# Optimization experiments

Measured on AMD Instinct MI355X. Metric: run time of the kernel, lower is better.

The kernel has to match this reference:

```python
import jax, jax.numpy as jnp
import numpy as np

B, I, O, N = 32, 512, 512, 16
XLO, XHI = 0.0, 1.0
SIGMA_INIT = (XHI - XLO) / N / 3.0
INV_SQRT2 = 0.7071067811865476


def setup_inputs() -> dict:
    key = jax.random.key(0)
    k0, k1, k2, k3, k4, k5 = jax.random.split(key, 6)
    x = jax.random.uniform(k0, (B, I), dtype=jnp.float32)  # inputs in xrange
    # learned parameters (perturbed around the module's init values so the
    # basis functions / gradients are non-degenerate)
    mx_train = 0.1 * jax.random.normal(k1, (I, O), dtype=jnp.float32)
    scale = 1.0 + 0.1 * jax.random.normal(k2, (I, O), dtype=jnp.float32)
    sigma = SIGMA_INIT * (1.0 + 0.1 * jax.random.normal(k3, (I, O, N), dtype=jnp.float32))
    alpha = 0.5 * jax.random.normal(k4, (I, O, N), dtype=jnp.float32)
    w = 0.001 * jax.random.normal(k5, (I, O, N), dtype=jnp.float32)
    # registered buffer: fixed basis centers
    mx_start = jnp.linspace(XLO, XHI, N, dtype=jnp.float32)  # (N,)
    return {"x": x, "mx_train": mx_train, "scale": scale, "sigma": sigma,
            "alpha": alpha, "w": w, "mx_start": mx_start}


def reference(x, mx_train, scale, sigma, alpha, w, mx_start):
    # z: (B, I, O, N) skewed/scaled basis argument
    centers = jnp.abs(scale)[:, :, None] * mx_start + mx_train[:, :, None]  # (I,O,N)
    z = (x[:, :, None, None] - centers[None]) / (jnp.abs(sigma) + 1e-8)
    # order == 1 branch: f = exp(-z^2) * 2*Phi(alpha*z); 2*Phi(u) = 1 + erf(u/sqrt(2))
    f = jnp.exp(-z * z) * (1.0 + jax.lax.erf(alpha * z * INV_SQRT2))
    # sum over input_dim (axis 1) and basis index n (axis 3)
    return jnp.einsum('bion,ion->bo', f, w)
```

## Files before the change

kernel.cpp:

```cpp
#include <hip/hip_runtime.h>
#include <math.h>

#define BB 32
#define II 512
#define OO 512
#define NN 16

#define NW 2
#define LOMAX (NN - NW)
#define QS 16
#define CHI 32
#define OPB 2
#define NOB (OO / OPB)

#if __has_builtin(__builtin_amdgcn_exp2f)
#define EXP2F(x) __builtin_amdgcn_exp2f(x)
#else
#define EXP2F(x) exp2f(x)
#endif
#if __has_builtin(__builtin_amdgcn_rcpf)
#define RCPF(x) __builtin_amdgcn_rcpf(x)
#else
#define RCPF(x) (1.0f / (x))
#endif

#define KS      1.2011224087f
#define K_A2N   0.5887050112f
#define EA1 0.278393f
#define EA2 0.230389f
#define EA3 0.000972f
#define EA4 0.078108f

__global__ __launch_bounds__(256, 8)
void kat_win(const float* __restrict__ x,
             const float* __restrict__ mx_train,
             const float* __restrict__ scale,
             const float* __restrict__ sigma,
             const float* __restrict__ alpha,
             const float* __restrict__ w,
             const float* __restrict__ mx_start,
             float* __restrict__ ws)
{
    __shared__ float4 pr[CHI * OPB * NN];
    __shared__ float  xs[BB * 33];
    __shared__ float2 sc[CHI * OPB];
    __shared__ float  red[OPB][8][BB];

    const int bid = blockIdx.x;
    const int ob  = bid & (NOB - 1);
    const int q   = bid >> 8;
    const int o0  = ob * OPB;
    const int tid = threadIdx.x;
    const int b   = tid & 31;
    const int iw  = tid >> 5;
    const int i0  = q * CHI;

#pragma unroll
    for (int p = 0; p < (BB * CHI) / 256; ++p) {
        const int idx = p * 256 + tid;
        const int bb  = idx >> 5;
        const int ii  = idx & 31;
        xs[bb * 33 + ii] = x[bb * II + i0 + ii];
    }
    {
        const int il = tid >> 3;
        const int r  = tid & 7;
        const int op = r >> 2;
        const int n0 = (r & 3) * 4;
        const int io = (i0 + il) * OO + o0 + op;
        const float4 sg4 = *reinterpret_cast<const float4*>(&sigma[io * NN + n0]);
        const float4 al4 = *reinterpret_cast<const float4*>(&alpha[io * NN + n0]);
        const float4 w4  = *reinterpret_cast<const float4*>(&w[io * NN + n0]);
        const float4 mx4 = *reinterpret_cast<const float4*>(&mx_start[n0]);
        const float  sca = fabsf(scale[io]);
        const float  mxt = mx_train[io];

        const float sg[4] = {sg4.x, sg4.y, sg4.z, sg4.w};
        const float al[4] = {al4.x, al4.y, al4.z, al4.w};
        const float wv[4] = {w4.x,  w4.y,  w4.z,  w4.w};
        const float mx[4] = {mx4.x, mx4.y, mx4.z, mx4.w};
        float4* dst = &pr[(il * OPB + op) * NN + n0];
#pragma unroll
        for (int c = 0; c < 4; ++c) {
            const float c1s = KS * RCPF(fabsf(sg[c]) + 1e-8f);
            const float ctr = fmaf(sca, mx[c], mxt);
            dst[c] = make_float4(c1s, -ctr * c1s, al[c] * K_A2N, wv[c]);
        }
    }
    if (tid < CHI * OPB) {
        const int ii  = tid >> 1;
        const int op  = tid & 1;
        const int io  = (i0 + ii) * OO + o0 + op;
        const float s   = fmaxf(fabsf(scale[io]), 1e-20f);
        const float inv = 15.0f * RCPF(s);
        sc[tid] = make_float2(inv, -mx_train[io] * inv);
    }
    __syncthreads();

    float acc0 = 0.0f, acc1 = 0.0f;
#pragma unroll
    for (int j = 0; j < CHI / 8; ++j) {
        const int ii = iw + 8 * j;
        const float xv = xs[b * 33 + ii];
#pragma unroll
        for (int op = 0; op < OPB; ++op) {
            const float2 s2 = sc[ii * OPB + op];
            const float  nc = fmaf(xv, s2.x, s2.y);
            const float lof = fminf(fmaxf(floorf(nc), 0.0f), (float)LOMAX);
            const int   lo  = (int)lof;
            const float4* pp = &pr[(ii * OPB + op) * NN + lo];
            float a = 0.0f;
#pragma unroll
            for (int k = 0; k < NW; ++k) {
                const float4 P = pp[k];
                const float zs = fmaf(xv, P.x, P.y);
                const float m  = -zs * zs;
                const float e  = EXP2F(m);
                const float u  = P.z * zs;
                const float au = fabsf(u);
                float d = fmaf(EA4, au, EA3);
                d = fmaf(d, au, EA2);
                d = fmaf(d, au, EA1);
                d = fmaf(d, au, 1.0f);
                const float r  = RCPF(d);
                const float r2 = r * r;
                const float r4 = r2 * r2;
                const float erfu = __builtin_copysignf(1.0f - r4, u);
                const float gg   = fmaf(e, erfu, e);
                a = fmaf(gg, P.w, a);
            }
            if (op == 0) acc0 += a; else acc1 += a;
        }
    }

    red[0][iw][b] = acc0;
    red[1][iw][b] = acc1;
    __syncthreads();
    if (tid < OPB * BB) {
        const int op = tid >> 5;
        const int bb = tid & 31;
        float s = 0.0f;
#pragma unroll
        for (int k = 0; k < 8; ++k) s += red[op][k][bb];
        ws[q * (BB * OO) + bb * OO + o0 + op] = s;
    }
}

__global__ __launch_bounds__(256)
void kat_reduce(const float* __restrict__ ws, float* __restrict__ out)
{
    const int idx = blockIdx.x * 256 + threadIdx.x;
    if (idx < BB * OO) {
        float s = 0.0f;
#pragma unroll
        for (int qq = 0; qq < QS; ++qq) s += ws[qq * (BB * OO) + idx];
        out[idx] = s;
    }
}

extern "C" void kernel_launch(void* const* d_in, const int* in_sizes, int n_in,
                              void* d_out, int out_size, void* d_ws, size_t ws_size,
                              hipStream_t stream)
{
    const float* x        = (const float*)d_in[0];
    const float* mx_train = (const float*)d_in[1];
    const float* scale    = (const float*)d_in[2];
    const float* sigma    = (const float*)d_in[3];
    const float* alpha    = (const float*)d_in[4];
    const float* w        = (const float*)d_in[5];
    const float* mx_start = (const float*)d_in[6];
    float* ws             = (float*)d_ws;
    float* out            = (float*)d_out;

    kat_win<<<QS * NOB, 256, 0, stream>>>(x, mx_train, scale, sigma,
                                          alpha, w, mx_start, ws);
    kat_reduce<<<(BB * OO + 255) / 256, 256, 0, stream>>>(ws, out);
}
```

Before: 22.17 us.

## Retile main kernel to 8 inputs by 8 outputs and transpose workspace layout

Each block of the main kernel now covers 8 inputs by 8 outputs instead of 32 inputs by 2 outputs. Each thread handles one input and accumulates eight outputs, so the sigma, alpha and w reads per input row become 512 contiguous bytes instead of 128. The number of input-chunk partial sums grows from 16 to 64. The workspace is stored output-major, and the reduce kernel is rewritten to read it coalesced and write the output with a stride. The gain is meant to come from better coalescing of the large parameter reads. The cost is four times more workspace traffic and a heavier second-pass reduction.

```diff
diff --git a/kernel.cpp b/kernel.cpp
--- a/kernel.cpp
+++ b/kernel.cpp
@@ -8,10 +8,11 @@
 
 #define NW 2
 #define LOMAX (NN - NW)
-#define QS 16
-#define CHI 32
-#define OPB 2
+#define OPB 8
+#define CHI 8
+#define QS (II / CHI)
 #define NOB (OO / OPB)
+#define XP (CHI + 1)
 
 #if __has_builtin(__builtin_amdgcn_exp2f)
 #define EXP2F(x) __builtin_amdgcn_exp2f(x)
@@ -31,7 +32,7 @@
 #define EA3 0.000972f
 #define EA4 0.078108f
 
-__global__ __launch_bounds__(256, 8)
+__global__ __launch_bounds__(256, 6)
 void kat_win(const float* __restrict__ x,
              const float* __restrict__ mx_train,
              const float* __restrict__ scale,
@@ -42,31 +43,28 @@
              float* __restrict__ ws)
 {
     __shared__ float4 pr[CHI * OPB * NN];
-    __shared__ float  xs[BB * 33];
+    __shared__ float  xs[BB * XP];
     __shared__ float2 sc[CHI * OPB];
     __shared__ float  red[OPB][8][BB];
 
     const int bid = blockIdx.x;
     const int ob  = bid & (NOB - 1);
-    const int q   = bid >> 8;
+    const int q   = bid >> 6;
     const int o0  = ob * OPB;
+    const int i0  = q * CHI;
     const int tid = threadIdx.x;
     const int b   = tid & 31;
     const int iw  = tid >> 5;
-    const int i0  = q * CHI;
 
-#pragma unroll
-    for (int p = 0; p < (BB * CHI) / 256; ++p) {
-        const int idx = p * 256 + tid;
-        const int bb  = idx >> 5;
-        const int ii  = idx & 31;
-        xs[bb * 33 + ii] = x[bb * II + i0 + ii];
+    {
+        const int bb = tid >> 3;
+        const int ii = tid & 7;
+        xs[bb * XP + ii] = x[bb * II + i0 + ii];
     }
     {
-        const int il = tid >> 3;
-        const int r  = tid & 7;
-        const int op = r >> 2;
-        const int n0 = (r & 3) * 4;
+        const int il = tid >> 5;
+        const int op = (tid >> 2) & 7;
+        const int n0 = (tid & 3) * 4;
         const int io = (i0 + il) * OO + o0 + op;
         const float4 sg4 = *reinterpret_cast<const float4*>(&sigma[io * NN + n0]);
         const float4 al4 = *reinterpret_cast<const float4*>(&alpha[io * NN + n0]);
@@ -88,74 +86,71 @@
         }
     }
     if (tid < CHI * OPB) {
-        const int ii  = tid >> 1;
-        const int op  = tid & 1;
-        const int io  = (i0 + ii) * OO + o0 + op;
+        const int ii = tid >> 3;
+        const int op = tid & 7;
+        const int io = (i0 + ii) * OO + o0 + op;
         const float s   = fmaxf(fabsf(scale[io]), 1e-20f);
         const float inv = 15.0f * RCPF(s);
-        sc[tid] = make_float2(inv, -mx_train[io] * inv);
+        sc[ii * OPB + op] = make_float2(inv, -mx_train[io] * inv);
     }
     __syncthreads();
 
-    float acc0 = 0.0f, acc1 = 0.0f;
+    float acc[OPB];
 #pragma unroll
-    for (int j = 0; j < CHI / 8; ++j) {
-        const int ii = iw + 8 * j;
-        const float xv = xs[b * 33 + ii];
+    for (int op = 0; op < OPB; ++op) acc[op] = 0.0f;
+
+    const float xv = xs[b * XP + iw];
 #pragma unroll
-        for (int op = 0; op < OPB; ++op) {
-            const float2 s2 = sc[ii * OPB + op];
-            const float  nc = fmaf(xv, s2.x, s2.y);
-            const float lof = fminf(fmaxf(floorf(nc), 0.0f), (float)LOMAX);
-            const int   lo  = (int)lof;
-            const float4* pp = &pr[(ii * OPB + op) * NN + lo];
-            float a = 0.0f;
+    for (int op = 0; op < OPB; ++op) {
+        const float2 s2 = sc[iw * OPB + op];
+        const float  nc = fmaf(xv, s2.x, s2.y);
+        const float lof = fminf(fmaxf(floorf(nc), 0.0f), (float)LOMAX);
+        const int   lo  = (int)lof;
+        const float4* pp = &pr[(iw * OPB + op) * NN + lo];
 #pragma unroll
-            for (int k = 0; k < NW; ++k) {
-                const float4 P = pp[k];
-                const float zs = fmaf(xv, P.x, P.y);
-                const float m  = -zs * zs;
-                const float e  = EXP2F(m);
-                const float u  = P.z * zs;
-                const float au = fabsf(u);
-                float d = fmaf(EA4, au, EA3);
-                d = fmaf(d, au, EA2);
-                d = fmaf(d, au, EA1);
-                d = fmaf(d, au, 1.0f);
-                const float r  = RCPF(d);
-                const float r2 = r * r;
-                const float r4 = r2 * r2;
-                const float erfu = __builtin_copysignf(1.0f - r4, u);
-                const float gg   = fmaf(e, erfu, e);
-                a = fmaf(gg, P.w, a);
-            }
-            if (op == 0) acc0 += a; else acc1 += a;
+        for (int k = 0; k < NW; ++k) {
+            const float4 P = pp[k];
+            const float zs = fmaf(xv, P.x, P.y);
+            const float m  = -zs * zs;
+            const float e  = EXP2F(m);
+            const float u  = P.z * zs;
+            const float au = fabsf(u);
+            float d = fmaf(EA4, au, EA3);
+            d = fmaf(d, au, EA2);
+            d = fmaf(d, au, EA1);
+            d = fmaf(d, au, 1.0f);
+            const float r  = RCPF(d);
+            const float r2 = r * r;
+            const float r4 = r2 * r2;
+            const float erfu = __builtin_copysignf(1.0f - r4, u);
+            const float gg   = fmaf(e, erfu, e);
+            acc[op] = fmaf(gg, P.w, acc[op]);
         }
     }
 
-    red[0][iw][b] = acc0;
-    red[1][iw][b] = acc1;
+#pragma unroll
+    for (int op = 0; op < OPB; ++op) red[op][iw][b] = acc[op];
     __syncthreads();
-    if (tid < OPB * BB) {
+    {
         const int op = tid >> 5;
         const int bb = tid & 31;
         float s = 0.0f;
 #pragma unroll
         for (int k = 0; k < 8; ++k) s += red[op][k][bb];
-        ws[q * (BB * OO) + bb * OO + o0 + op] = s;
+        ws[q * (OO * BB) + (o0 + op) * BB + bb] = s;
     }
 }
 
 __global__ __launch_bounds__(256)
 void kat_reduce(const float* __restrict__ ws, float* __restrict__ out)
 {
-    const int idx = blockIdx.x * 256 + threadIdx.x;
-    if (idx < BB * OO) {
-        float s = 0.0f;
+    const int tid = threadIdx.x;
+    const int o   = blockIdx.x * 8 + (tid >> 5);
+    const int bb  = tid & 31;
+    float s = 0.0f;
 #pragma unroll
-        for (int qq = 0; qq < QS; ++qq) s += ws[qq * (BB * OO) + idx];
-        out[idx] = s;
-    }
+    for (int qq = 0; qq < QS; ++qq) s += ws[qq * (OO * BB) + o * BB + bb];
+    out[bb * OO + o] = s;
 }
 
 extern "C" void kernel_launch(void* const* d_in, const int* in_sizes, int n_in,
@@ -174,5 +169,5 @@
 
     kat_win<<<QS * NOB, 256, 0, stream>>>(x, mx_train, scale, sigma,
                                           alpha, w, mx_start, ws);
-    kat_reduce<<<(BB * OO + 255) / 256, 256, 0, stream>>>(ws, out);
+    kat_reduce<<<OO / 8, 256, 0, stream>>>(ws, out);
 }
```

Measured after the change: 35.10 us. +58.3%, slower.
